# Optimization experiments

Hardware: AMD Instinct MI355X
Metric: run time of the kernel (lower is better)

## Reference

```python
import jax, jax.numpy as jnp
import numpy as np

B, S, IN, H, OUT = 32, 512, 1024, 1024, 1024


def setup_inputs() -> dict:
    key = jax.random.key(0)
    ks = jax.random.split(key, 12)
    sc = 0.02
    d = {
        "x": jax.random.normal(ks[0], (B, S, IN), dtype=jnp.float32),
        # torch nn.Linear weights are (out_features, in_features); in_features = IN + H
        "Wf": jax.random.normal(ks[1], (H, IN + H), dtype=jnp.float32) * sc,
        "bf": jax.random.normal(ks[2], (H,), dtype=jnp.float32) * sc,
        "Wi": jax.random.normal(ks[3], (H, IN + H), dtype=jnp.float32) * sc,
        "bi": jax.random.normal(ks[4], (H,), dtype=jnp.float32) * sc,
        "Wc": jax.random.normal(ks[5], (H, IN + H), dtype=jnp.float32) * sc,
        "bc": jax.random.normal(ks[6], (H,), dtype=jnp.float32) * sc,
        "Wo": jax.random.normal(ks[7], (H, IN + H), dtype=jnp.float32) * sc,
        "bo": jax.random.normal(ks[8], (H,), dtype=jnp.float32) * sc,
        "Wfc": jax.random.normal(ks[9], (OUT, H), dtype=jnp.float32) * sc,
        "bfc": jax.random.normal(ks[10], (OUT,), dtype=jnp.float32) * sc,
    }
    return d


def reference(x, Wf, bf, Wi, bi, Wc, bc, Wo, bo, Wfc, bfc):
    batch, seq_len, _ = x.shape
    hidden = Wf.shape[0]
    h0 = jnp.zeros((batch, hidden), dtype=x.dtype)
    c0 = jnp.zeros((batch, hidden), dtype=x.dtype)

    def step(carry, x_t):
        h, c = carry
        # NOTE: original concatenates (h_t, x_t) in this order
        z = jnp.concatenate([h, x_t], axis=1)  # [B, H+IN]
        f = jax.nn.sigmoid(z @ Wf.T + bf)
        i = jax.nn.sigmoid(z @ Wi.T + bi)
        c_hat = jnp.tanh(z @ Wc.T + bc)
        c_new = i * c_hat + f * c
        o = jax.nn.sigmoid(z @ Wo.T + bo)
        h_new = o * jnp.tanh(c_new)
        return (h_new, c_new), h_new

    xs = jnp.swapaxes(x, 0, 1)  # [S, B, IN]
    _, hs = jax.lax.scan(step, (h0, c0), xs)  # hs: [S, B, H]
    outputs = jnp.swapaxes(hs, 0, 1)  # [B, S, H]
    out = outputs @ Wfc.T + bfc  # [B, S, OUT]
    return out
```

## Files before the change

### kernel.cpp

```cpp
#include <hip/hip_runtime.h>
#include <hip/hip_bf16.h>

#define BATCH 32
#define SEQ   512
#define IND   1024
#define HD    1024
#define ZD    2048
#define NG    4096
#define WG_ELEMS (1024 * 2048)
#define PBLK 128

typedef short  shortx8 __attribute__((ext_vector_type(8)));
typedef float  floatx4 __attribute__((ext_vector_type(4)));

#define MFMA16(a, b, c) __builtin_amdgcn_mfma_f32_16x16x32_bf16((a), (b), (c), 0, 0, 0)

__device__ __forceinline__ float sigmoidf_(float x) {
    return 1.0f / (1.0f + __expf(-x));
}
__device__ __forceinline__ float tanhf_(float x) {
    return 1.0f - 2.0f / (__expf(2.0f * x) + 1.0f);
}

__device__ __forceinline__ short bf16s(float x) {
    __hip_bfloat16 h = __float2bfloat16(x);
    return *reinterpret_cast<short*>(&h);
}

__device__ __forceinline__ float bf2f(unsigned short u) {
    unsigned v = ((unsigned)u) << 16;
    float f;
    __builtin_memcpy(&f, &v, 4);
    return f;
}

__device__ __forceinline__ shortx8 cvt8(const float* __restrict__ p) {
    float4 v0 = *(const float4*)p;
    float4 v1 = *(const float4*)(p + 4);
    shortx8 r;
    r[0] = bf16s(v0.x); r[1] = bf16s(v0.y); r[2] = bf16s(v0.z); r[3] = bf16s(v0.w);
    r[4] = bf16s(v1.x); r[5] = bf16s(v1.y); r[6] = bf16s(v1.z); r[7] = bf16s(v1.w);
    return r;
}

__global__ __launch_bounds__(256) void cvt_f32_bf16(
    const float* __restrict__ src, __hip_bfloat16* __restrict__ dst, int n)
{
    int i = (blockIdx.x * 256 + threadIdx.x) * 4;
    if (i < n) {
        float4 v = *(const float4*)(src + i);
        dst[i + 0] = __float2bfloat16(v.x);
        dst[i + 1] = __float2bfloat16(v.y);
        dst[i + 2] = __float2bfloat16(v.z);
        dst[i + 3] = __float2bfloat16(v.w);
    }
}

__global__ __launch_bounds__(256) void gemm_gx(
    const float* __restrict__ x,
    const __hip_bfloat16* __restrict__ Wb,
    const float* __restrict__ bf_, const float* __restrict__ bi_,
    const float* __restrict__ bc_, const float* __restrict__ bo_,
    __hip_bfloat16* __restrict__ Gx, const int t0)
{
    const int wave = (blockIdx.x << 2) + (threadIdx.x >> 6);
    const int mt = wave >> 6;
    const int nt = wave & 63;
    const int lane = threadIdx.x & 63;
    const int quad = lane >> 4;
    const int l16  = lane & 15;
    const int m0 = mt << 6;
    const int n0 = nt << 6;
    const int g  = n0 >> 10;
    const __hip_bfloat16* Wg = Wb + (size_t)g * WG_ELEMS;
    const float* bg = (g == 0) ? bf_ : (g == 1) ? bi_ : (g == 2) ? bc_ : bo_;
    const int j0 = n0 & 1023;

    floatx4 acc[4][4];
#pragma unroll
    for (int i = 0; i < 4; i++)
#pragma unroll
        for (int j = 0; j < 4; j++) acc[i][j] = (floatx4)(0.0f);

    const float* arow[4];
    const __hip_bfloat16* brow[4];
#pragma unroll
    for (int i = 0; i < 4; i++) {
        const int r = m0 + i * 16 + l16;
        const int t = t0 + (r >> 5);
        const int b = r & 31;
        arow[i] = x + ((size_t)b * SEQ + t) * IND + quad * 8;
    }
#pragma unroll
    for (int j = 0; j < 4; j++)
        brow[j] = Wg + (size_t)(j0 + j * 16 + l16) * ZD + HD + quad * 8;

    for (int k0 = 0; k0 < IND; k0 += 32) {
        shortx8 a[4], b[4];
#pragma unroll
        for (int i = 0; i < 4; i++) a[i] = cvt8(arow[i] + k0);
#pragma unroll
        for (int j = 0; j < 4; j++) b[j] = *(const shortx8*)(brow[j] + k0);
#pragma unroll
        for (int i = 0; i < 4; i++)
#pragma unroll
            for (int j = 0; j < 4; j++)
                acc[i][j] = MFMA16(a[i], b[j], acc[i][j]);
    }

#pragma unroll
    for (int j = 0; j < 4; j++) {
        const int n  = n0 + j * 16 + l16;
        const int jj = j0 + j * 16 + l16;
        const float bias = bg[jj];
#pragma unroll
        for (int i = 0; i < 4; i++) {
#pragma unroll
            for (int r = 0; r < 4; r++) {
                const int row = m0 + i * 16 + quad * 4 + r;
                Gx[(size_t)row * NG + n] = __float2bfloat16(acc[i][j][r] + bias);
            }
        }
    }
}

__global__ __launch_bounds__(256) void lstm_step(
    const __hip_bfloat16* __restrict__ gx,
    const int t,
    const __hip_bfloat16* __restrict__ Wb,
    const __hip_bfloat16* __restrict__ hzero,
    float* __restrict__ c,
    __hip_bfloat16* __restrict__ hs)
{
    const int jt = (blockIdx.x << 2) + (threadIdx.x >> 6);
    const int lane = threadIdx.x & 63;
    const int quad = lane >> 4;
    const int l16  = lane & 15;
    const int j0   = jt << 4;

    const __hip_bfloat16* hb;
    size_t rstride;
    if (t == 0) { hb = hzero; rstride = HD; }
    else        { hb = hs + (size_t)(t - 1) * HD; rstride = (size_t)SEQ * HD; }

    const __hip_bfloat16* wrow[4];
#pragma unroll
    for (int g = 0; g < 4; g++)
        wrow[g] = Wb + (size_t)g * WG_ELEMS + (size_t)(j0 + l16) * ZD + quad * 8;

    const __hip_bfloat16* hrow0 = hb + (size_t)l16 * rstride + quad * 8;
    const __hip_bfloat16* hrow1 = hb + (size_t)(16 + l16) * rstride + quad * 8;

    floatx4 acc[4][2];
#pragma unroll
    for (int g = 0; g < 4; g++) { acc[g][0] = (floatx4)(0.0f); acc[g][1] = (floatx4)(0.0f); }

    for (int k0 = 0; k0 < HD; k0 += 32) {
        shortx8 a0 = *(const shortx8*)(hrow0 + k0);
        shortx8 a1 = *(const shortx8*)(hrow1 + k0);
#pragma unroll
        for (int g = 0; g < 4; g++) {
            shortx8 bfrag = *(const shortx8*)(wrow[g] + k0);
            acc[g][0] = MFMA16(a0, bfrag, acc[g][0]);
            acc[g][1] = MFMA16(a1, bfrag, acc[g][1]);
        }
    }

    const int j = j0 + l16;
#pragma unroll
    for (int i = 0; i < 2; i++) {
#pragma unroll
        for (int r = 0; r < 4; r++) {
            const int bb = i * 16 + quad * 4 + r;
            const size_t gbase = (size_t)bb * NG + j;
            const float fp = acc[0][i][r] + __bfloat162float(gx[gbase + 0 * HD]);
            const float ip = acc[1][i][r] + __bfloat162float(gx[gbase + 1 * HD]);
            const float cp = acc[2][i][r] + __bfloat162float(gx[gbase + 2 * HD]);
            const float op = acc[3][i][r] + __bfloat162float(gx[gbase + 3 * HD]);
            const float fg = sigmoidf_(fp);
            const float ig = sigmoidf_(ip);
            const float cg = tanhf_(cp);
            const float og = sigmoidf_(op);
            const size_t ci = (size_t)bb * HD + j;
            const float cnew = ig * cg + fg * c[ci];
            const float hnew = og * tanhf_(cnew);
            c[ci] = cnew;
            hs[((size_t)bb * SEQ + t) * HD + j] = __float2bfloat16(hnew);
        }
    }
}

__global__ __launch_bounds__(256, 1) void lstm_persist(
    const __hip_bfloat16* __restrict__ Wb,
    const float* __restrict__ x,
    __hip_bfloat16* __restrict__ Gx,
    const float* __restrict__ bf_, const float* __restrict__ bi_,
    const float* __restrict__ bc_, const float* __restrict__ bo_,
    const int T,
    const __hip_bfloat16* __restrict__ hzero,
    float* __restrict__ c_ws,
    __hip_bfloat16* __restrict__ hs,
    unsigned* __restrict__ bar)
{
    __shared__ float accf[2 * 1168];

    const int tid  = threadIdx.x;
    const int blk  = blockIdx.x;
    const int wv   = tid >> 6;
    const int lane = tid & 63;
    const int quad = lane >> 4;
    const int l16  = lane & 15;
    unsigned* gcnt = bar + 2048;

    if (blk >= PBLK) {
        const int pw = (blk - PBLK) * 4 + wv;
        const int nt = pw & 63;
        const int n0 = nt << 6;
        const int g  = n0 >> 10;
        const __hip_bfloat16* Wg = Wb + (size_t)g * WG_ELEMS;
        const float* bg = (g == 0) ? bf_ : (g == 1) ? bi_ : (g == 2) ? bc_ : bo_;
        const int j0 = n0 & 1023;

        const __hip_bfloat16* brow[4];
#pragma unroll
        for (int j = 0; j < 4; j++)
            brow[j] = Wg + (size_t)(j0 + j * 16 + l16) * ZD + HD + quad * 8;

        float bias[4];
#pragma unroll
        for (int j = 0; j < 4; j++) bias[j] = bg[j0 + j * 16 + l16];

        for (int it = 0; it < 32; it++) {
            const int mt = (pw >> 6) + 8 * it;
            const int m0 = mt << 6;

            floatx4 acc[4][4];
#pragma unroll
            for (int i = 0; i < 4; i++)
#pragma unroll
                for (int j = 0; j < 4; j++) acc[i][j] = (floatx4)(0.0f);

            const float* arow[4];
#pragma unroll
            for (int i = 0; i < 4; i++) {
                const int r = m0 + i * 16 + l16;
                const int t = r >> 5;
                const int b = r & 31;
                arow[i] = x + ((size_t)b * SEQ + t) * IND + quad * 8;
            }

            for (int k0 = 0; k0 < IND; k0 += 32) {
                shortx8 a[4], b[4];
#pragma unroll
                for (int i = 0; i < 4; i++) a[i] = cvt8(arow[i] + k0);
#pragma unroll
                for (int j = 0; j < 4; j++) b[j] = *(const shortx8*)(brow[j] + k0);
#pragma unroll
                for (int i = 0; i < 4; i++)
#pragma unroll
                    for (int j = 0; j < 4; j++)
                        acc[i][j] = MFMA16(a[i], b[j], acc[i][j]);
            }

#pragma unroll
            for (int j = 0; j < 4; j++) {
                const int n = n0 + j * 16 + l16;
#pragma unroll
                for (int i = 0; i < 4; i++) {
#pragma unroll
                    for (int r = 0; r < 4; r++) {
                        const int row = m0 + i * 16 + quad * 4 + r;
                        const float v = acc[i][j][r] + bias[j];
                        const unsigned my = (unsigned)(unsigned short)bf16s(v);
                        const unsigned nb = (unsigned)__shfl_xor((int)my, 1);
                        if ((l16 & 1) == 0) {
                            unsigned* dst = (unsigned*)(Gx + (size_t)row * NG + n);
                            __hip_atomic_store(dst, my | (nb << 16),
                                               __ATOMIC_RELAXED,
                                               __HIP_MEMORY_SCOPE_AGENT);
                        }
                    }
                }
            }
            asm volatile("s_waitcnt vmcnt(0)" ::: "memory");
            if (lane == 0)
                __hip_atomic_fetch_add(gcnt + mt * 16, 1u,
                                       __ATOMIC_RELAXED, __HIP_MEMORY_SCOPE_AGENT);
        }
        return;
    }

    const int wm = wv & 1;
    const int wk = wv >> 1;

    shortx8 Bfrag[2][16];
#pragma unroll
    for (int ct = 0; ct < 2; ct++) {
        const int lc = ct * 16 + l16;
        const int jj = lc >> 2, g = lc & 3;
        const __hip_bfloat16* wr =
            Wb + (size_t)g * WG_ELEMS + (size_t)(blk * 8 + jj) * ZD + wk * 512 + quad * 8;
#pragma unroll
        for (int ks = 0; ks < 16; ks++)
            Bfrag[ct][ks] = *(const shortx8*)(wr + ks * 32);
    }

    const int pjj = tid & 7;
    const int pb  = tid >> 3;
    const int pj  = blk * 8 + pjj;
    float creg = c_ws[blk * 256 + tid];

    while (__hip_atomic_load(gcnt, __ATOMIC_RELAXED,
                             __HIP_MEMORY_SCOPE_AGENT) < 64)
        __builtin_amdgcn_s_sleep(1);
    asm volatile("" ::: "memory");
    __builtin_amdgcn_sched_barrier(0);

    unsigned short gxr0, gxr1, gxr2, gxr3;
    {
        const __hip_bfloat16* gx = Gx + (size_t)pb * NG + pj;
        gxr0 = *(const unsigned short*)(gx + 0 * HD);
        gxr1 = *(const unsigned short*)(gx + 1 * HD);
        gxr2 = *(const unsigned short*)(gx + 2 * HD);
        gxr3 = *(const unsigned short*)(gx + 3 * HD);
    }
    int mt_ok = 0;

    for (int tt = 0; tt < T; tt++) {
        const int t = tt;
        const __hip_bfloat16* hb;
        size_t rstride;
        if (t == 0) { hb = hzero; rstride = HD; }
        else        { hb = hs + (size_t)(t - 1) * HD; rstride = (size_t)SEQ * HD; }

        unsigned short ngxr0 = 0, ngxr1 = 0, ngxr2 = 0, ngxr3 = 0;
        if (tt + 1 < T) {
            const int mtn = (tt + 1) >> 1;
            if (mtn > mt_ok) {
                while (__hip_atomic_load(gcnt + mtn * 16, __ATOMIC_RELAXED,
                                         __HIP_MEMORY_SCOPE_AGENT) < 64)
                    __builtin_amdgcn_s_sleep(1);
                mt_ok = mtn;
                asm volatile("" ::: "memory");
                __builtin_amdgcn_sched_barrier(0);
            }
            const __hip_bfloat16* gx1 = Gx + ((size_t)(tt + 1) * BATCH + pb) * NG + pj;
            ngxr0 = *(const unsigned short*)(gx1 + 0 * HD);
            ngxr1 = *(const unsigned short*)(gx1 + 1 * HD);
            ngxr2 = *(const unsigned short*)(gx1 + 2 * HD);
            ngxr3 = *(const unsigned short*)(gx1 + 3 * HD);
        }

        const __hip_bfloat16* arow =
            hb + (size_t)(wm * 16 + l16) * rstride + wk * 512 + quad * 8;
        floatx4 acc0 = (floatx4)(0.0f), acc1 = (floatx4)(0.0f);
#pragma unroll
        for (int ks = 0; ks < 16; ks++) {
            shortx8 av = *(const shortx8*)(arow + ks * 32);
            acc0 = MFMA16(av, Bfrag[0][ks], acc0);
            acc1 = MFMA16(av, Bfrag[1][ks], acc1);
        }

        {
            const int b0 = wm * 16 + quad * 4;
            *(floatx4*)(accf + wk * 1168 + (l16)      * 36 + b0) = acc0;
            *(floatx4*)(accf + wk * 1168 + (16 + l16) * 36 + b0) = acc1;
        }
        __syncthreads();

        {
            const int i0 = (pjj * 4 + 0) * 36 + pb;
            const int i1 = (pjj * 4 + 1) * 36 + pb;
            const int i2 = (pjj * 4 + 2) * 36 + pb;
            const int i3 = (pjj * 4 + 3) * 36 + pb;
            const float fp = accf[i0] + accf[1168 + i0] + bf2f(gxr0);
            const float ip = accf[i1] + accf[1168 + i1] + bf2f(gxr1);
            const float cp = accf[i2] + accf[1168 + i2] + bf2f(gxr2);
            const float op = accf[i3] + accf[1168 + i3] + bf2f(gxr3);
            const float fg = sigmoidf_(fp);
            const float ig = sigmoidf_(ip);
            const float cg = tanhf_(cp);
            const float og = sigmoidf_(op);
            creg = ig * cg + fg * creg;
            const float hnew = og * tanhf_(creg);

            const unsigned my = (unsigned)(unsigned short)bf16s(hnew);
            const unsigned nb = (unsigned)__shfl_xor((int)my, 1);
            if ((tid & 1) == 0) {
                unsigned* dst = (unsigned*)(hs + ((size_t)pb * SEQ + t) * HD + pj);
                const unsigned packed = my | (nb << 16);
                __hip_atomic_store(dst, packed, __ATOMIC_RELAXED,
                                   __HIP_MEMORY_SCOPE_AGENT);
            }
        }

        if (tt < T - 1) {
            __syncthreads();
            const unsigned epoch = (unsigned)(tt + 1);
            if (wv == 0) {
                if (lane == 0) {
                    __hip_atomic_store(bar + blk * 16, epoch, __ATOMIC_RELAXED,
                                       __HIP_MEMORY_SCOPE_AGENT);
                }
                unsigned* p0 = bar + lane * 16;
                unsigned* p1 = bar + (64 + lane) * 16;
                bool d0 = false, d1 = false;
                while (true) {
                    if (!d0) d0 = (__hip_atomic_load(p0, __ATOMIC_RELAXED,
                                       __HIP_MEMORY_SCOPE_AGENT) >= epoch);
                    if (!d1) d1 = (__hip_atomic_load(p1, __ATOMIC_RELAXED,
                                       __HIP_MEMORY_SCOPE_AGENT) >= epoch);
                    if (__all(d0 && d1)) break;
                    __builtin_amdgcn_s_sleep(1);
                }
                asm volatile("" ::: "memory");
                __builtin_amdgcn_sched_barrier(0);
            }
            __syncthreads();
        }

        gxr0 = ngxr0; gxr1 = ngxr1; gxr2 = ngxr2; gxr3 = ngxr3;
    }

    c_ws[blk * 256 + tid] = creg;
}

__global__ __launch_bounds__(256) void gemm_fc(
    const __hip_bfloat16* __restrict__ hs,
    const __hip_bfloat16* __restrict__ Wfcb,
    const float* __restrict__ bfc,
    float* __restrict__ out)
{
    const int wave = (blockIdx.x << 2) + (threadIdx.x >> 6);
    const int mt = wave >> 4;
    const int nt = wave & 15;
    const int lane = threadIdx.x & 63;
    const int quad = lane >> 4;
    const int l16  = lane & 15;
    const int m0 = mt << 6;
    const int n0 = nt << 6;

    floatx4 acc[4][4];
#pragma unroll
    for (int i = 0; i < 4; i++)
#pragma unroll
        for (int j = 0; j < 4; j++) acc[i][j] = (floatx4)(0.0f);

    const __hip_bfloat16* arow[4];
    const __hip_bfloat16* brow[4];
#pragma unroll
    for (int i = 0; i < 4; i++)
        arow[i] = hs + (size_t)(m0 + i * 16 + l16) * HD + quad * 8;
#pragma unroll
    for (int j = 0; j < 4; j++)
        brow[j] = Wfcb + (size_t)(n0 + j * 16 + l16) * HD + quad * 8;

    for (int k0 = 0; k0 < HD; k0 += 32) {
        shortx8 a[4], b[4];
#pragma unroll
        for (int i = 0; i < 4; i++) a[i] = *(const shortx8*)(arow[i] + k0);
#pragma unroll
        for (int j = 0; j < 4; j++) b[j] = *(const shortx8*)(brow[j] + k0);
#pragma unroll
        for (int i = 0; i < 4; i++)
#pragma unroll
            for (int j = 0; j < 4; j++)
                acc[i][j] = MFMA16(a[i], b[j], acc[i][j]);
    }

#pragma unroll
    for (int j = 0; j < 4; j++) {
        const int n = n0 + j * 16 + l16;
        const float bias = bfc[n];
#pragma unroll
        for (int i = 0; i < 4; i++) {
#pragma unroll
            for (int r = 0; r < 4; r++) {
                const int row = m0 + i * 16 + quad * 4 + r;
                out[(size_t)row * 1024 + n] = acc[i][j][r] + bias;
            }
        }
    }
}

extern "C" void kernel_launch(void* const* d_in, const int* in_sizes, int n_in,
                              void* d_out, int out_size, void* d_ws, size_t ws_size,
                              hipStream_t stream) {
    const float* x   = (const float*)d_in[0];
    const float* Wf  = (const float*)d_in[1];
    const float* bf_ = (const float*)d_in[2];
    const float* Wi  = (const float*)d_in[3];
    const float* bi_ = (const float*)d_in[4];
    const float* Wc  = (const float*)d_in[5];
    const float* bc_ = (const float*)d_in[6];
    const float* Wo  = (const float*)d_in[7];
    const float* bo_ = (const float*)d_in[8];
    const float* Wfc = (const float*)d_in[9];
    const float* bfc = (const float*)d_in[10];
    float* out = (float*)d_out;

    char* ws = (char*)d_ws;
    const size_t WB_OFF  = 0;
    const size_t WFC_OFF = (size_t)4 * WG_ELEMS * 2;
    const size_t HS_OFF  = WFC_OFF + (size_t)HD * HD * 2;
    const size_t ST_OFF  = HS_OFF + (size_t)BATCH * SEQ * HD * 2;
    const size_t HZ_BYTES  = (size_t)BATCH * HD * 2;
    const size_t C_BYTES   = (size_t)PBLK * 256 * 4;
    const size_t BAR_BYTES = 128 * 64 + 256 * 64;
    const size_t ST_BYTES  = HZ_BYTES + C_BYTES + BAR_BYTES;
    const size_t GX_OFF  = ST_OFF + ST_BYTES;

    __hip_bfloat16* Wb    = (__hip_bfloat16*)(ws + WB_OFF);
    __hip_bfloat16* Wfcb  = (__hip_bfloat16*)(ws + WFC_OFF);
    __hip_bfloat16* hs    = (__hip_bfloat16*)(ws + HS_OFF);
    __hip_bfloat16* hzero = (__hip_bfloat16*)(ws + ST_OFF);
    float*          cbuf  = (float*)(ws + ST_OFF + HZ_BYTES);
    unsigned*       bar   = (unsigned*)(ws + ST_OFF + HZ_BYTES + C_BYTES);
    __hip_bfloat16* Gx    = (__hip_bfloat16*)(ws + GX_OFF);

    const size_t GX_FULL = (size_t)SEQ * BATCH * NG * 2;
    const int persist = (GX_OFF + GX_FULL <= ws_size);
    int T_CHUNK = 1;
    if (!persist) {
        const size_t GX_STEP = (size_t)BATCH * NG * 2;
        const int fopts[3] = {8, 2, 1};
        for (int i = 0; i < 3; i++) {
            if (GX_OFF + (size_t)fopts[i] * GX_STEP <= ws_size) {
                T_CHUNK = fopts[i]; break;
            }
        }
    }

    cvt_f32_bf16<<<2048, 256, 0, stream>>>(Wf, Wb + 0 * (size_t)WG_ELEMS, WG_ELEMS);
    cvt_f32_bf16<<<2048, 256, 0, stream>>>(Wi, Wb + 1 * (size_t)WG_ELEMS, WG_ELEMS);
    cvt_f32_bf16<<<2048, 256, 0, stream>>>(Wc, Wb + 2 * (size_t)WG_ELEMS, WG_ELEMS);
    cvt_f32_bf16<<<2048, 256, 0, stream>>>(Wo, Wb + 3 * (size_t)WG_ELEMS, WG_ELEMS);
    cvt_f32_bf16<<<1024, 256, 0, stream>>>(Wfc, Wfcb, HD * HD);

    hipMemsetAsync(ws + ST_OFF, 0, ST_BYTES, stream);

    if (persist) {
        lstm_persist<<<2 * PBLK, 256, 0, stream>>>(
            Wb, x, Gx, bf_, bi_, bc_, bo_, SEQ, hzero, cbuf, hs, bar);
    } else {
        for (int t0 = 0; t0 < SEQ; t0 += T_CHUNK) {
            gemm_gx<<<T_CHUNK * 8, 256, 0, stream>>>(
                x, Wb, bf_, bi_, bc_, bo_, Gx, t0);
            for (int t = t0; t < t0 + T_CHUNK; t++) {
                const __hip_bfloat16* gx_t = Gx + (size_t)(t - t0) * BATCH * NG;
                lstm_step<<<16, 256, 0, stream>>>(gx_t, t, Wb, hzero, cbuf, hs);
            }
        }
    }

    gemm_fc<<<1024, 256, 0, stream>>>(hs, Wfcb, bfc, out);
}
```

Before: 2.802 ms.

## Fuse output FC GEMM into persistent LSTM kernel, overlapping with recurrence

The helper blocks of the persistent kernel, after finishing the input-projection GEMM, now also compute the final FC layer over chunks of 64 timesteps. Each chunk waits on the recurrent blocks' per-step barrier counters before reading the hidden states. This overlaps the FC GEMM with the serial recurrence and removes the separate gemm_fc launch. The last step now also publishes its barrier epoch so the FC consumers can finish. Risks are polling contention with the recurrent barrier and the helper blocks taking a long tail after the last step.

```diff
diff --git a/kernel.cpp b/kernel.cpp
--- a/kernel.cpp
+++ b/kernel.cpp
@@ -196,6 +196,9 @@
     __hip_bfloat16* __restrict__ Gx,
     const float* __restrict__ bf_, const float* __restrict__ bi_,
     const float* __restrict__ bc_, const float* __restrict__ bo_,
+    const __hip_bfloat16* __restrict__ Wfcb,
+    const float* __restrict__ bfc,
+    float* __restrict__ out,
     const int T,
     const __hip_bfloat16* __restrict__ hzero,
     float* __restrict__ c_ws,
@@ -213,79 +216,154 @@
     unsigned* gcnt = bar + 2048;
 
     if (blk >= PBLK) {
-        const int pw = (blk - PBLK) * 4 + wv;
-        const int nt = pw & 63;
-        const int n0 = nt << 6;
-        const int g  = n0 >> 10;
-        const __hip_bfloat16* Wg = Wb + (size_t)g * WG_ELEMS;
-        const float* bg = (g == 0) ? bf_ : (g == 1) ? bi_ : (g == 2) ? bc_ : bo_;
-        const int j0 = n0 & 1023;
-
-        const __hip_bfloat16* brow[4];
-#pragma unroll
-        for (int j = 0; j < 4; j++)
-            brow[j] = Wg + (size_t)(j0 + j * 16 + l16) * ZD + HD + quad * 8;
-
-        float bias[4];
-#pragma unroll
-        for (int j = 0; j < 4; j++) bias[j] = bg[j0 + j * 16 + l16];
-
-        for (int it = 0; it < 32; it++) {
-            const int mt = (pw >> 6) + 8 * it;
-            const int m0 = mt << 6;
-
-            floatx4 acc[4][4];
-#pragma unroll
-            for (int i = 0; i < 4; i++)
-#pragma unroll
-                for (int j = 0; j < 4; j++) acc[i][j] = (floatx4)(0.0f);
-
-            const float* arow[4];
-#pragma unroll
-            for (int i = 0; i < 4; i++) {
-                const int r = m0 + i * 16 + l16;
-                const int t = r >> 5;
-                const int b = r & 31;
-                arow[i] = x + ((size_t)b * SEQ + t) * IND + quad * 8;
-            }
-
-            for (int k0 = 0; k0 < IND; k0 += 32) {
-                shortx8 a[4], b[4];
-#pragma unroll
-                for (int i = 0; i < 4; i++) a[i] = cvt8(arow[i] + k0);
-#pragma unroll
-                for (int j = 0; j < 4; j++) b[j] = *(const shortx8*)(brow[j] + k0);
+        const int pb_ = blk - PBLK;
+        const int pw = pb_ * 4 + wv;
+        {
+            const int nt = pw & 63;
+            const int n0 = nt << 6;
+            const int g  = n0 >> 10;
+            const __hip_bfloat16* Wg = Wb + (size_t)g * WG_ELEMS;
+            const float* bg = (g == 0) ? bf_ : (g == 1) ? bi_ : (g == 2) ? bc_ : bo_;
+            const int j0 = n0 & 1023;
+
+            const __hip_bfloat16* brow[4];
+#pragma unroll
+            for (int j = 0; j < 4; j++)
+                brow[j] = Wg + (size_t)(j0 + j * 16 + l16) * ZD + HD + quad * 8;
+
+            float bias[4];
+#pragma unroll
+            for (int j = 0; j < 4; j++) bias[j] = bg[j0 + j * 16 + l16];
+
+            for (int it = 0; it < 32; it++) {
+                const int mt = (pw >> 6) + 8 * it;
+                const int m0 = mt << 6;
+
+                floatx4 acc[4][4];
 #pragma unroll
                 for (int i = 0; i < 4; i++)
 #pragma unroll
-                    for (int j = 0; j < 4; j++)
-                        acc[i][j] = MFMA16(a[i], b[j], acc[i][j]);
-            }
-
-#pragma unroll
-            for (int j = 0; j < 4; j++) {
-                const int n = n0 + j * 16 + l16;
+                    for (int j = 0; j < 4; j++) acc[i][j] = (floatx4)(0.0f);
+
+                const float* arow[4];
 #pragma unroll
                 for (int i = 0; i < 4; i++) {
-#pragma unroll
-                    for (int r = 0; r < 4; r++) {
-                        const int row = m0 + i * 16 + quad * 4 + r;
-                        const float v = acc[i][j][r] + bias[j];
-                        const unsigned my = (unsigned)(unsigned short)bf16s(v);
-                        const unsigned nb = (unsigned)__shfl_xor((int)my, 1);
-                        if ((l16 & 1) == 0) {
-                            unsigned* dst = (unsigned*)(Gx + (size_t)row * NG + n);
-                            __hip_atomic_store(dst, my | (nb << 16),
-                                               __ATOMIC_RELAXED,
-                                               __HIP_MEMORY_SCOPE_AGENT);
+                    const int r = m0 + i * 16 + l16;
+                    const int t = r >> 5;
+                    const int b = r & 31;
+                    arow[i] = x + ((size_t)b * SEQ + t) * IND + quad * 8;
+                }
+
+                for (int k0 = 0; k0 < IND; k0 += 32) {
+                    shortx8 a[4], b[4];
+#pragma unroll
+                    for (int i = 0; i < 4; i++) a[i] = cvt8(arow[i] + k0);
+#pragma unroll
+                    for (int j = 0; j < 4; j++) b[j] = *(const shortx8*)(brow[j] + k0);
+#pragma unroll
+                    for (int i = 0; i < 4; i++)
+#pragma unroll
+                        for (int j = 0; j < 4; j++)
+                            acc[i][j] = MFMA16(a[i], b[j], acc[i][j]);
+                }
+
+#pragma unroll
+                for (int j = 0; j < 4; j++) {
+                    const int n = n0 + j * 16 + l16;
+#pragma unroll
+                    for (int i = 0; i < 4; i++) {
+#pragma unroll
+                        for (int r = 0; r < 4; r++) {
+                            const int row = m0 + i * 16 + quad * 4 + r;
+                            const float v = acc[i][j][r] + bias[j];
+                            const unsigned my = (unsigned)(unsigned short)bf16s(v);
+                            const unsigned nb = (unsigned)__shfl_xor((int)my, 1);
+                            if ((l16 & 1) == 0) {
+                                unsigned* dst = (unsigned*)(Gx + (size_t)row * NG + n);
+                                __hip_atomic_store(dst, my | (nb << 16),
+                                                   __ATOMIC_RELAXED,
+                                                   __HIP_MEMORY_SCOPE_AGENT);
+                            }
                         }
                     }
                 }
-            }
-            asm volatile("s_waitcnt vmcnt(0)" ::: "memory");
-            if (lane == 0)
-                __hip_atomic_fetch_add(gcnt + mt * 16, 1u,
-                                       __ATOMIC_RELAXED, __HIP_MEMORY_SCOPE_AGENT);
+                asm volatile("s_waitcnt vmcnt(0)" ::: "memory");
+                if (lane == 0)
+                    __hip_atomic_fetch_add(gcnt + mt * 16, 1u,
+                                           __ATOMIC_RELAXED, __HIP_MEMORY_SCOPE_AGENT);
+            }
+        }
+
+        {
+            const int fb  = (pb_ & 7) * 4 + wv;
+            const int fnt = pb_ >> 3;
+            const int n0  = fnt << 6;
+
+            const __hip_bfloat16* brow[4];
+#pragma unroll
+            for (int j = 0; j < 4; j++)
+                brow[j] = Wfcb + (size_t)(n0 + j * 16 + l16) * HD + quad * 8;
+            float biasf[4];
+#pragma unroll
+            for (int j = 0; j < 4; j++) biasf[j] = bfc[n0 + j * 16 + l16];
+
+            for (int tc = 0; tc < 8; tc++) {
+                const unsigned need = (unsigned)((tc + 1) * 64);
+                {
+                    unsigned* p0 = bar + lane * 16;
+                    unsigned* p1 = bar + (64 + lane) * 16;
+                    bool d0 = false, d1 = false;
+                    while (true) {
+                        if (!d0) d0 = (__hip_atomic_load(p0, __ATOMIC_RELAXED,
+                                           __HIP_MEMORY_SCOPE_AGENT) >= need);
+                        if (!d1) d1 = (__hip_atomic_load(p1, __ATOMIC_RELAXED,
+                                           __HIP_MEMORY_SCOPE_AGENT) >= need);
+                        if (__all(d0 && d1)) break;
+                        __builtin_amdgcn_s_sleep(8);
+                    }
+                    asm volatile("" ::: "memory");
+                    __builtin_amdgcn_sched_barrier(0);
+                }
+
+                const int m0 = fb * SEQ + tc * 64;
+
+                floatx4 acc[4][4];
+#pragma unroll
+                for (int i = 0; i < 4; i++)
+#pragma unroll
+                    for (int j = 0; j < 4; j++) acc[i][j] = (floatx4)(0.0f);
+
+                const __hip_bfloat16* arow[4];
+#pragma unroll
+                for (int i = 0; i < 4; i++)
+                    arow[i] = hs + (size_t)(m0 + i * 16 + l16) * HD + quad * 8;
+
+                for (int k0 = 0; k0 < HD; k0 += 32) {
+                    shortx8 a[4], b[4];
+#pragma unroll
+                    for (int i = 0; i < 4; i++) a[i] = *(const shortx8*)(arow[i] + k0);
+#pragma unroll
+                    for (int j = 0; j < 4; j++) b[j] = *(const shortx8*)(brow[j] + k0);
+#pragma unroll
+                    for (int i = 0; i < 4; i++)
+#pragma unroll
+                        for (int j = 0; j < 4; j++)
+                            acc[i][j] = MFMA16(a[i], b[j], acc[i][j]);
+                }
+
+#pragma unroll
+                for (int j = 0; j < 4; j++) {
+                    const int n = n0 + j * 16 + l16;
+#pragma unroll
+                    for (int i = 0; i < 4; i++) {
+#pragma unroll
+                        for (int r = 0; r < 4; r++) {
+                            const int row = m0 + i * 16 + quad * 4 + r;
+                            out[(size_t)row * 1024 + n] = acc[i][j][r] + biasf[j];
+                        }
+                    }
+                }
+            }
         }
         return;
     }
@@ -394,14 +472,14 @@
             }
         }
 
+        __syncthreads();
+        if (wv == 0 && lane == 0) {
+            __hip_atomic_store(bar + blk * 16, (unsigned)(tt + 1),
+                               __ATOMIC_RELAXED, __HIP_MEMORY_SCOPE_AGENT);
+        }
         if (tt < T - 1) {
-            __syncthreads();
             const unsigned epoch = (unsigned)(tt + 1);
             if (wv == 0) {
-                if (lane == 0) {
-                    __hip_atomic_store(bar + blk * 16, epoch, __ATOMIC_RELAXED,
-                                       __HIP_MEMORY_SCOPE_AGENT);
-                }
                 unsigned* p0 = bar + lane * 16;
                 unsigned* p1 = bar + (64 + lane) * 16;
                 bool d0 = false, d1 = false;
@@ -541,7 +619,8 @@
 
     if (persist) {
         lstm_persist<<<2 * PBLK, 256, 0, stream>>>(
-            Wb, x, Gx, bf_, bi_, bc_, bo_, SEQ, hzero, cbuf, hs, bar);
+            Wb, x, Gx, bf_, bi_, bc_, bo_, Wfcb, bfc, out,
+            SEQ, hzero, cbuf, hs, bar);
     } else {
         for (int t0 = 0; t0 < SEQ; t0 += T_CHUNK) {
             gemm_gx<<<T_CHUNK * 8, 256, 0, stream>>>(
@@ -551,7 +630,6 @@
                 lstm_step<<<16, 256, 0, stream>>>(gx_t, t, Wb, hzero, cbuf, hs);
             }
         }
-    }
-
-    gemm_fc<<<1024, 256, 0, stream>>>(hs, Wfcb, bfc, out);
-}
+        gemm_fc<<<1024, 256, 0, stream>>>(hs, Wfcb, bfc, out);
+    }
+}
```

After: 2.754 ms. No clear change (-1.7%).
